# Kernel tuning notes

Hardware: AMD Instinct MI355X
Metric: run time of the kernel (lower is better)

The kernel has to match this reference:

```python
import jax, jax.numpy as jnp
import numpy as np

UP = 2


def _lpf_rect(N, cutoff):
    # ideal lowpass rect over full-FFT frequency axis (with Nyquist 0.5 fix)
    cutoff_low = int((N * cutoff) // 2)
    cutoff_high = int(N - cutoff_low)
    rect = np.ones(N, dtype=np.float32)
    rect[cutoff_low + 1:cutoff_high] = 0.0
    if (N * cutoff) % 2 == 0:
        rect[cutoff_low] = 0.5
        rect[cutoff_high] = 0.5
    return rect


def _recon_rect(N, cutoff):
    # reconstruction rect for zero-insertion upsampling (no Nyquist halving)
    cutoff_low = int((N * cutoff) // 2)
    cutoff_high = int(N - cutoff_low)
    rect = np.ones(N, dtype=np.float32)
    rect[cutoff_low + 1:cutoff_high] = 0.0
    return rect


def _rfft2_mask(rect_h, rect_w):
    # outer product mask on rfft2 grid: full H axis x half W axis
    half_w = rect_w.shape[0] // 2 + 1
    return jnp.asarray(rect_h[:, None] * rect_w[None, :half_w])


def setup_inputs() -> dict:
    key = jax.random.key(0)
    x = jax.random.normal(key, (32, 128, 64, 64), dtype=jnp.float32)
    # PolyAct default init_coef (buffer, non-trainable)
    coef = jnp.array([0.0169394634313126, 0.5, 0.3078363963999393, 0.0],
                     dtype=jnp.float32)
    return {"x": x, "coef": coef}


def reference(x, coef):
    B, C, H, W = x.shape
    Hu, Wu = H * UP, W * UP

    # ---- UpsampleRFFT: zero-insertion then ideal reconstruction filter ----
    xu = jnp.zeros((B, C, Hu, Wu), x.dtype).at[:, :, ::UP, ::UP].set(x)
    recon_mask = _rfft2_mask(_recon_rect(Hu, 1.0 / UP), _recon_rect(Wu, 1.0 / UP))
    f = jnp.fft.rfft2(xu) * (UP * UP) * recon_mask
    xu = jnp.fft.irfft2(f, s=(Hu, Wu))

    # ---- PolyAct: calc_polynomial loops range(2, deg) with deg=3, so only
    # terms up to x^2 are used (coef[3] is never applied) ----
    y = coef[0] + coef[1] * xu + coef[2] * xu * xu

    # ---- LPF_RFFT with cutoff = 1/up ----
    lpf_mask = _rfft2_mask(_lpf_rect(Hu, 1.0 / UP), _lpf_rect(Wu, 1.0 / UP))
    y = jnp.fft.irfft2(jnp.fft.rfft2(y) * lpf_mask, s=(Hu, Wu))

    # ---- decimate back to original resolution ----
    return y[:, :, ::UP, ::UP]
```

## Files before the change

### kernel.cpp

```cpp
#include <hip/hip_runtime.h>
#include <math.h>


typedef short short8 __attribute__((ext_vector_type(8)));
typedef float f32x16 __attribute__((ext_vector_type(16)));

#define LSH 68

__device__ __forceinline__ short f2bf(float f) {
  unsigned u = __float_as_uint(f);
  u += 0x7FFFu + ((u >> 16) & 1u);
  return (short)(u >> 16);
}
__device__ __forceinline__ float bf2f(short s) {
  return __uint_as_float(((unsigned)(unsigned short)s) << 16);
}
__device__ __forceinline__ short8 ldrow(const short* p) {
  union { unsigned u[4]; short8 s; } v;
  const uint2 lo = *(const uint2*)p;
  const uint2 hi = *(const uint2*)(p + 4);
  v.u[0] = lo.x; v.u[1] = lo.y; v.u[2] = hi.x; v.u[3] = hi.y;
  return v.s;
}

__global__ __launch_bounds__(256, 3) void uppolyact_kernel(
    const float* __restrict__ x, const float* __restrict__ coef,
    float* __restrict__ out) {
  __shared__ __align__(16) short Xr[64 * LSH];
  __shared__ __align__(16) short XcZ[64 * LSH];
  __shared__ __align__(16) short LrU[64 * LSH];
  __shared__ __align__(16) short Zoo[64 * LSH];
  __shared__ __align__(16) short ftab[16 * 64 * 8];
  __shared__ float g64[64];
  __shared__ float tvec[64], uvec[64], sRv[64], Luv[64];
  __shared__ float sigv;

  const int tid = threadIdx.x;
  const int lane = tid & 63;
  const int w = tid >> 6;
  const int q = lane >> 5;
  const int l31 = lane & 31;
  const int rb = w >> 1, cb = w & 1;
  const size_t base = (size_t)blockIdx.x * 4096;

  if (tid < 64) {
    const int d = 2 * tid + 1;
    float s = 1.0f;
    for (int k = 1; k <= 32; ++k) {
      const int qq = (k * d) & 127;
      s += 2.0f * cosf((float)M_PI * (1.0f / 64.0f) * (float)qq);
    }
    g64[tid] = s * (1.0f / 64.0f);
  }
  {
    const float4* xv = (const float4*)(x + base);
#pragma unroll
    for (int e = 0; e < 4; ++e) {
      const int k4 = tid + 256 * e;
      const float4 v = xv[k4];
      const int r = k4 >> 4, c = (k4 & 15) << 2;
      const short b0 = f2bf(v.x), b1 = f2bf(v.y), b2 = f2bf(v.z), b3 = f2bf(v.w);
      short* pr = &Xr[r * LSH + c];
      pr[0] = b0; pr[1] = b1; pr[2] = b2; pr[3] = b3;
      XcZ[(c + 0) * LSH + r] = b0;
      XcZ[(c + 1) * LSH + r] = b1;
      XcZ[(c + 2) * LSH + r] = b2;
      XcZ[(c + 3) * LSH + r] = b3;
    }
  }
  __syncthreads();

#pragma unroll
  for (int e = 0; e < 4; ++e) {
    const int entry = tid + 256 * e;
    const int s_ = entry >> 6, ln = entry & 63;
    const int t_ = s_ >> 3, blk = (s_ >> 2) & 1, kk = s_ & 3;
    const int basei = kk * 16 + (ln >> 5) * 8 - (ln & 31) - 32 * blk;
    short* dst = &ftab[(s_ * 64 + ln) * 8];
#pragma unroll
    for (int j = 0; j < 8; ++j) {
      const int i0 = basei + j;
      const int idx = t_ ? ((-i0) & 63) : (i0 & 63);
      dst[j] = f2bf(g64[idx]);
    }
  }
  if (tid < 64) {
    float acc = 0.0f;
    for (int i = 0; i < 64; ++i) {
      const float xv_ = bf2f(XcZ[tid * LSH + i]);
      acc += (i & 1) ? -xv_ : xv_;
    }
    tvec[tid] = acc;
  } else if (tid < 128) {
    const int i = tid - 64;
    float acc = 0.0f;
    for (int j = 0; j < 64; ++j) {
      const float xv_ = bf2f(Xr[i * LSH + j]);
      acc += (j & 1) ? -xv_ : xv_;
    }
    uvec[i] = acc;
  }
  __syncthreads();

  if (tid < 64) {
    float acc = 0.0f;
    for (int m = 0; m < 64; ++m) acc += tvec[m] * g64[(tid - m) & 63];
    sRv[tid] = acc;
  } else if (tid < 128) {
    const int i = tid - 64;
    float acc = 0.0f;
    for (int m = 0; m < 64; ++m) acc += g64[(i - m) & 63] * uvec[m];
    Luv[i] = acc;
  } else if (tid == 128) {
    float acc = 0.0f;
    for (int i = 0; i < 64; ++i) acc += (i & 1) ? -uvec[i] : uvec[i];
    sigv = acc;
  }

  f32x16 Rt, Lt;
#pragma unroll
  for (int r = 0; r < 16; ++r) { Rt[r] = 0.0f; Lt[r] = 0.0f; }
#pragma unroll
  for (int kk = 0; kk < 4; ++kk) {
    const short8 aR = *(const short8*)&ftab[(((2 + rb) * 4 + kk) * 64 + lane) * 8];
    const short8 bR = ldrow(&Xr[(cb * 32 + l31) * LSH + kk * 16 + q * 8]);
    Rt = __builtin_amdgcn_mfma_f32_32x32x16_bf16(aR, bR, Rt, 0, 0, 0);
    const short8 aL = ldrow(&XcZ[(rb * 32 + l31) * LSH + kk * 16 + q * 8]);
    const short8 bL = *(const short8*)&ftab[(((2 + cb) * 4 + kk) * 64 + lane) * 8];
    Lt = __builtin_amdgcn_mfma_f32_32x32x16_bf16(aL, bL, Lt, 0, 0, 0);
  }
  __syncthreads();

  float zoe[16];
#pragma unroll
  for (int r = 0; r < 16; ++r) {
    const int jrow = rb * 32 + (r & 3) + 4 * q + 8 * (r >> 2);
    const int icol = cb * 32 + l31;
    const float sgi = (icol & 1) ? -1.0f : 1.0f;
    const float sgj = (jrow & 1) ? -1.0f : 1.0f;
    const float veo = Rt[r] + sgi * sRv[jrow] * (1.0f / 64.0f);
    XcZ[icol * LSH + jrow] = f2bf(veo * veo);
    LrU[icol * LSH + jrow] = f2bf(Lt[r]);
    const float voe = Lt[r] + Luv[icol] * sgj * (1.0f / 64.0f);
    zoe[r] = voe * voe;
  }
  __syncthreads();

  f32x16 OOt;
#pragma unroll
  for (int r = 0; r < 16; ++r) OOt[r] = 0.0f;
#pragma unroll
  for (int kk = 0; kk < 4; ++kk) {
    const short8 a = *(const short8*)&ftab[(((2 + rb) * 4 + kk) * 64 + lane) * 8];
    const short8 b = ldrow(&LrU[(cb * 32 + l31) * LSH + kk * 16 + q * 8]);
    OOt = __builtin_amdgcn_mfma_f32_32x32x16_bf16(a, b, OOt, 0, 0, 0);
  }
#pragma unroll
  for (int r = 0; r < 16; ++r) {
    const int jrow = rb * 32 + (r & 3) + 4 * q + 8 * (r >> 2);
    const int icol = cb * 32 + l31;
    Zoo[icol * LSH + jrow] = f2bf(OOt[r] * OOt[r]);
  }
  __syncthreads();

  f32x16 Ut, Wv;
#pragma unroll
  for (int r = 0; r < 16; ++r) { Ut[r] = zoe[r]; Wv[r] = 0.0f; }
#pragma unroll
  for (int kk = 0; kk < 4; ++kk) {
    const short8 aU = *(const short8*)&ftab[(((0 + rb) * 4 + kk) * 64 + lane) * 8];
    const short8 bU = ldrow(&Zoo[(cb * 32 + l31) * LSH + kk * 16 + q * 8]);
    Ut = __builtin_amdgcn_mfma_f32_32x32x16_bf16(aU, bU, Ut, 0, 0, 0);
    const short8 aW = ldrow(&XcZ[(rb * 32 + l31) * LSH + kk * 16 + q * 8]);
    const short8 bW = *(const short8*)&ftab[(((0 + cb) * 4 + kk) * 64 + lane) * 8];
    Wv = __builtin_amdgcn_mfma_f32_32x32x16_bf16(aW, bW, Wv, 0, 0, 0);
  }
#pragma unroll
  for (int r = 0; r < 16; ++r) {
    const int jrow = rb * 32 + (r & 3) + 4 * q + 8 * (r >> 2);
    const int icol = cb * 32 + l31;
    LrU[jrow * LSH + icol] = f2bf(Ut[r]);
  }
  __syncthreads();

  f32x16 Vv;
#pragma unroll
  for (int r = 0; r < 16; ++r) Vv[r] = 0.0f;
#pragma unroll
  for (int kk = 0; kk < 4; ++kk) {
    const short8 a = *(const short8*)&ftab[(((0 + rb) * 4 + kk) * 64 + lane) * 8];
    const short8 b = ldrow(&LrU[(cb * 32 + l31) * LSH + kk * 16 + q * 8]);
    Vv = __builtin_amdgcn_mfma_f32_32x32x16_bf16(a, b, Vv, 0, 0, 0);
  }

  const float c0 = coef[0], c1 = coef[1];
  const float c2q = 0.25f * coef[2];
  const float* xb = x + base;
  float* ob = out + base;
#pragma unroll
  for (int r = 0; r < 16; ++r) {
    const int irow = rb * 32 + (r & 3) + 4 * q + 8 * (r >> 2);
    const int jcol = cb * 32 + l31;
    const float sgi = (irow & 1) ? -1.0f : 1.0f;
    const float sgj = (jcol & 1) ? -1.0f : 1.0f;
    const float xv_ = bf2f(Xr[irow * LSH + jcol]);
    const float vee = xv_ + (sgi * tvec[jcol] + uvec[irow] * sgj) * (1.0f / 64.0f) +
                      sgi * sgj * sigv * (1.0f / 4096.0f);
    const float zee = vee * vee;
    const float xg = xb[irow * 64 + jcol];
    ob[irow * 64 + jcol] = c0 + c1 * xg + c2q * (zee + Vv[r] + Wv[r]);
  }
}

extern "C" void kernel_launch(void* const* d_in, const int* in_sizes, int n_in,
                              void* d_out, int out_size, void* d_ws,
                              size_t ws_size, hipStream_t stream) {
  const float* x = (const float*)d_in[0];
  const float* coef = (const float*)d_in[1];
  float* out = (float*)d_out;
  const int channels = out_size / 4096;
  uppolyact_kernel<<<dim3(channels), dim3(256), 0, stream>>>(x, coef, out);
}
```

Measured before the change: 150.4 us.

## Make kernel persistent over channels and parallelize per-channel reductions

The kernel becomes grid-stride persistent: at most 1024 blocks loop over the 4096 channels, so the g64 and ftab twiddle-table setup is paid once per block instead of once per channel. The alternating-sign row and column sums and the circular convolutions are spread across all 256 threads with shuffle reductions, where before only 64 to 128 threads did serial loops. sigv is now computed from tvec through a wave reduction, and the t/u sums overlap with the first MFMA stage. In exchange, each block runs long sequential chains, which can reduce latency hiding between blocks.

```diff
diff --git a/kernel.cpp b/kernel.cpp
--- a/kernel.cpp
+++ b/kernel.cpp
@@ -25,7 +25,7 @@
 
 __global__ __launch_bounds__(256, 3) void uppolyact_kernel(
     const float* __restrict__ x, const float* __restrict__ coef,
-    float* __restrict__ out) {
+    float* __restrict__ out, int nch) {
   __shared__ __align__(16) short Xr[64 * LSH];
   __shared__ __align__(16) short XcZ[64 * LSH];
   __shared__ __align__(16) short LrU[64 * LSH];
@@ -41,7 +41,6 @@
   const int q = lane >> 5;
   const int l31 = lane & 31;
   const int rb = w >> 1, cb = w & 1;
-  const size_t base = (size_t)blockIdx.x * 4096;
 
   if (tid < 64) {
     const int d = 2 * tid + 1;
@@ -52,22 +51,6 @@
     }
     g64[tid] = s * (1.0f / 64.0f);
   }
-  {
-    const float4* xv = (const float4*)(x + base);
-#pragma unroll
-    for (int e = 0; e < 4; ++e) {
-      const int k4 = tid + 256 * e;
-      const float4 v = xv[k4];
-      const int r = k4 >> 4, c = (k4 & 15) << 2;
-      const short b0 = f2bf(v.x), b1 = f2bf(v.y), b2 = f2bf(v.z), b3 = f2bf(v.w);
-      short* pr = &Xr[r * LSH + c];
-      pr[0] = b0; pr[1] = b1; pr[2] = b2; pr[3] = b3;
-      XcZ[(c + 0) * LSH + r] = b0;
-      XcZ[(c + 1) * LSH + r] = b1;
-      XcZ[(c + 2) * LSH + r] = b2;
-      XcZ[(c + 3) * LSH + r] = b3;
-    }
-  }
   __syncthreads();
 
 #pragma unroll
@@ -84,131 +67,167 @@
       dst[j] = f2bf(g64[idx]);
     }
   }
-  if (tid < 64) {
-    float acc = 0.0f;
-    for (int i = 0; i < 64; ++i) {
-      const float xv_ = bf2f(XcZ[tid * LSH + i]);
-      acc += (i & 1) ? -xv_ : xv_;
-    }
-    tvec[tid] = acc;
-  } else if (tid < 128) {
-    const int i = tid - 64;
-    float acc = 0.0f;
-    for (int j = 0; j < 64; ++j) {
-      const float xv_ = bf2f(Xr[i * LSH + j]);
-      acc += (j & 1) ? -xv_ : xv_;
-    }
-    uvec[i] = acc;
-  }
-  __syncthreads();
-
-  if (tid < 64) {
-    float acc = 0.0f;
-    for (int m = 0; m < 64; ++m) acc += tvec[m] * g64[(tid - m) & 63];
-    sRv[tid] = acc;
-  } else if (tid < 128) {
-    const int i = tid - 64;
-    float acc = 0.0f;
-    for (int m = 0; m < 64; ++m) acc += g64[(i - m) & 63] * uvec[m];
-    Luv[i] = acc;
-  } else if (tid == 128) {
-    float acc = 0.0f;
-    for (int i = 0; i < 64; ++i) acc += (i & 1) ? -uvec[i] : uvec[i];
-    sigv = acc;
-  }
-
-  f32x16 Rt, Lt;
-#pragma unroll
-  for (int r = 0; r < 16; ++r) { Rt[r] = 0.0f; Lt[r] = 0.0f; }
-#pragma unroll
-  for (int kk = 0; kk < 4; ++kk) {
-    const short8 aR = *(const short8*)&ftab[(((2 + rb) * 4 + kk) * 64 + lane) * 8];
-    const short8 bR = ldrow(&Xr[(cb * 32 + l31) * LSH + kk * 16 + q * 8]);
-    Rt = __builtin_amdgcn_mfma_f32_32x32x16_bf16(aR, bR, Rt, 0, 0, 0);
-    const short8 aL = ldrow(&XcZ[(rb * 32 + l31) * LSH + kk * 16 + q * 8]);
-    const short8 bL = *(const short8*)&ftab[(((2 + cb) * 4 + kk) * 64 + lane) * 8];
-    Lt = __builtin_amdgcn_mfma_f32_32x32x16_bf16(aL, bL, Lt, 0, 0, 0);
-  }
-  __syncthreads();
-
-  float zoe[16];
-#pragma unroll
-  for (int r = 0; r < 16; ++r) {
-    const int jrow = rb * 32 + (r & 3) + 4 * q + 8 * (r >> 2);
-    const int icol = cb * 32 + l31;
-    const float sgi = (icol & 1) ? -1.0f : 1.0f;
-    const float sgj = (jrow & 1) ? -1.0f : 1.0f;
-    const float veo = Rt[r] + sgi * sRv[jrow] * (1.0f / 64.0f);
-    XcZ[icol * LSH + jrow] = f2bf(veo * veo);
-    LrU[icol * LSH + jrow] = f2bf(Lt[r]);
-    const float voe = Lt[r] + Luv[icol] * sgj * (1.0f / 64.0f);
-    zoe[r] = voe * voe;
-  }
-  __syncthreads();
-
-  f32x16 OOt;
-#pragma unroll
-  for (int r = 0; r < 16; ++r) OOt[r] = 0.0f;
-#pragma unroll
-  for (int kk = 0; kk < 4; ++kk) {
-    const short8 a = *(const short8*)&ftab[(((2 + rb) * 4 + kk) * 64 + lane) * 8];
-    const short8 b = ldrow(&LrU[(cb * 32 + l31) * LSH + kk * 16 + q * 8]);
-    OOt = __builtin_amdgcn_mfma_f32_32x32x16_bf16(a, b, OOt, 0, 0, 0);
-  }
-#pragma unroll
-  for (int r = 0; r < 16; ++r) {
-    const int jrow = rb * 32 + (r & 3) + 4 * q + 8 * (r >> 2);
-    const int icol = cb * 32 + l31;
-    Zoo[icol * LSH + jrow] = f2bf(OOt[r] * OOt[r]);
-  }
-  __syncthreads();
-
-  f32x16 Ut, Wv;
-#pragma unroll
-  for (int r = 0; r < 16; ++r) { Ut[r] = zoe[r]; Wv[r] = 0.0f; }
-#pragma unroll
-  for (int kk = 0; kk < 4; ++kk) {
-    const short8 aU = *(const short8*)&ftab[(((0 + rb) * 4 + kk) * 64 + lane) * 8];
-    const short8 bU = ldrow(&Zoo[(cb * 32 + l31) * LSH + kk * 16 + q * 8]);
-    Ut = __builtin_amdgcn_mfma_f32_32x32x16_bf16(aU, bU, Ut, 0, 0, 0);
-    const short8 aW = ldrow(&XcZ[(rb * 32 + l31) * LSH + kk * 16 + q * 8]);
-    const short8 bW = *(const short8*)&ftab[(((0 + cb) * 4 + kk) * 64 + lane) * 8];
-    Wv = __builtin_amdgcn_mfma_f32_32x32x16_bf16(aW, bW, Wv, 0, 0, 0);
-  }
-#pragma unroll
-  for (int r = 0; r < 16; ++r) {
-    const int jrow = rb * 32 + (r & 3) + 4 * q + 8 * (r >> 2);
-    const int icol = cb * 32 + l31;
-    LrU[jrow * LSH + icol] = f2bf(Ut[r]);
-  }
-  __syncthreads();
-
-  f32x16 Vv;
-#pragma unroll
-  for (int r = 0; r < 16; ++r) Vv[r] = 0.0f;
-#pragma unroll
-  for (int kk = 0; kk < 4; ++kk) {
-    const short8 a = *(const short8*)&ftab[(((0 + rb) * 4 + kk) * 64 + lane) * 8];
-    const short8 b = ldrow(&LrU[(cb * 32 + l31) * LSH + kk * 16 + q * 8]);
-    Vv = __builtin_amdgcn_mfma_f32_32x32x16_bf16(a, b, Vv, 0, 0, 0);
-  }
 
   const float c0 = coef[0], c1 = coef[1];
   const float c2q = 0.25f * coef[2];
-  const float* xb = x + base;
-  float* ob = out + base;
-#pragma unroll
-  for (int r = 0; r < 16; ++r) {
-    const int irow = rb * 32 + (r & 3) + 4 * q + 8 * (r >> 2);
-    const int jcol = cb * 32 + l31;
-    const float sgi = (irow & 1) ? -1.0f : 1.0f;
-    const float sgj = (jcol & 1) ? -1.0f : 1.0f;
-    const float xv_ = bf2f(Xr[irow * LSH + jcol]);
-    const float vee = xv_ + (sgi * tvec[jcol] + uvec[irow] * sgj) * (1.0f / 64.0f) +
-                      sgi * sgj * sigv * (1.0f / 4096.0f);
-    const float zee = vee * vee;
-    const float xg = xb[irow * 64 + jcol];
-    ob[irow * 64 + jcol] = c0 + c1 * xg + c2q * (zee + Vv[r] + Wv[r]);
+
+  for (int ch = blockIdx.x; ch < nch; ch += gridDim.x) {
+    const size_t base = (size_t)ch * 4096;
+    const float* xb = x + base;
+    float* ob = out + base;
+
+    __syncthreads();
+
+    {
+      const float4* xv = (const float4*)xb;
+#pragma unroll
+      for (int e = 0; e < 4; ++e) {
+        const int k4 = tid + 256 * e;
+        const float4 v = xv[k4];
+        const int r = k4 >> 4, c = (k4 & 15) << 2;
+        const short b0 = f2bf(v.x), b1 = f2bf(v.y), b2 = f2bf(v.z), b3 = f2bf(v.w);
+        short* pr = &Xr[r * LSH + c];
+        pr[0] = b0; pr[1] = b1; pr[2] = b2; pr[3] = b3;
+        XcZ[(c + 0) * LSH + r] = b0;
+        XcZ[(c + 1) * LSH + r] = b1;
+        XcZ[(c + 2) * LSH + r] = b2;
+        XcZ[(c + 3) * LSH + r] = b3;
+      }
+    }
+    __syncthreads();
+
+    {
+      const int o = tid >> 1, h = tid & 1;
+      const short* src = (o < 64) ? &XcZ[o * LSH + 32 * h]
+                                  : &Xr[(o - 64) * LSH + 32 * h];
+      float acc = 0.0f;
+#pragma unroll
+      for (int p = 0; p < 4; ++p) {
+        const short8 v = ldrow(src + 8 * p);
+#pragma unroll
+        for (int j = 0; j < 8; ++j) {
+          const float f = bf2f(v[j]);
+          acc += (j & 1) ? -f : f;
+        }
+      }
+      acc += __shfl_xor(acc, 1);
+      if (h == 0) {
+        if (o < 64) tvec[o] = acc; else uvec[o - 64] = acc;
+      }
+    }
+
+    f32x16 Rt, Lt;
+#pragma unroll
+    for (int r = 0; r < 16; ++r) { Rt[r] = 0.0f; Lt[r] = 0.0f; }
+#pragma unroll
+    for (int kk = 0; kk < 4; ++kk) {
+      const short8 aR = *(const short8*)&ftab[(((2 + rb) * 4 + kk) * 64 + lane) * 8];
+      const short8 bR = ldrow(&Xr[(cb * 32 + l31) * LSH + kk * 16 + q * 8]);
+      Rt = __builtin_amdgcn_mfma_f32_32x32x16_bf16(aR, bR, Rt, 0, 0, 0);
+      const short8 aL = ldrow(&XcZ[(rb * 32 + l31) * LSH + kk * 16 + q * 8]);
+      const short8 bL = *(const short8*)&ftab[(((2 + cb) * 4 + kk) * 64 + lane) * 8];
+      Lt = __builtin_amdgcn_mfma_f32_32x32x16_bf16(aL, bL, Lt, 0, 0, 0);
+    }
+    __syncthreads();
+
+    {
+      const int o = tid >> 1, h = tid & 1;
+      const int o63 = o & 63;
+      const float* vsrc = (o < 64) ? tvec : uvec;
+      float acc = 0.0f;
+#pragma unroll
+      for (int p = 0; p < 32; ++p) {
+        const int m = 32 * h + p;
+        acc += vsrc[m] * g64[(o63 - m) & 63];
+      }
+      acc += __shfl_xor(acc, 1);
+      if (h == 0) {
+        if (o < 64) sRv[o] = acc; else Luv[o - 64] = acc;
+      }
+    }
+    if (w == 0) {
+      float sv = (lane & 1) ? -tvec[lane] : tvec[lane];
+#pragma unroll
+      for (int d_ = 1; d_ < 64; d_ <<= 1) sv += __shfl_xor(sv, d_);
+      if (lane == 0) sigv = sv;
+    }
+    __syncthreads();
+
+    float zoe[16];
+#pragma unroll
+    for (int r = 0; r < 16; ++r) {
+      const int jrow = rb * 32 + (r & 3) + 4 * q + 8 * (r >> 2);
+      const int icol = cb * 32 + l31;
+      const float sgi = (icol & 1) ? -1.0f : 1.0f;
+      const float sgj = (jrow & 1) ? -1.0f : 1.0f;
+      const float veo = Rt[r] + sgi * sRv[jrow] * (1.0f / 64.0f);
+      XcZ[icol * LSH + jrow] = f2bf(veo * veo);
+      LrU[icol * LSH + jrow] = f2bf(Lt[r]);
+      const float voe = Lt[r] + Luv[icol] * sgj * (1.0f / 64.0f);
+      zoe[r] = voe * voe;
+    }
+    __syncthreads();
+
+    f32x16 OOt;
+#pragma unroll
+    for (int r = 0; r < 16; ++r) OOt[r] = 0.0f;
+#pragma unroll
+    for (int kk = 0; kk < 4; ++kk) {
+      const short8 a = *(const short8*)&ftab[(((2 + rb) * 4 + kk) * 64 + lane) * 8];
+      const short8 b = ldrow(&LrU[(cb * 32 + l31) * LSH + kk * 16 + q * 8]);
+      OOt = __builtin_amdgcn_mfma_f32_32x32x16_bf16(a, b, OOt, 0, 0, 0);
+    }
+#pragma unroll
+    for (int r = 0; r < 16; ++r) {
+      const int jrow = rb * 32 + (r & 3) + 4 * q + 8 * (r >> 2);
+      const int icol = cb * 32 + l31;
+      Zoo[icol * LSH + jrow] = f2bf(OOt[r] * OOt[r]);
+    }
+    __syncthreads();
+
+    f32x16 Ut, Wv;
+#pragma unroll
+    for (int r = 0; r < 16; ++r) { Ut[r] = zoe[r]; Wv[r] = 0.0f; }
+#pragma unroll
+    for (int kk = 0; kk < 4; ++kk) {
+      const short8 aU = *(const short8*)&ftab[(((0 + rb) * 4 + kk) * 64 + lane) * 8];
+      const short8 bU = ldrow(&Zoo[(cb * 32 + l31) * LSH + kk * 16 + q * 8]);
+      Ut = __builtin_amdgcn_mfma_f32_32x32x16_bf16(aU, bU, Ut, 0, 0, 0);
+      const short8 aW = ldrow(&XcZ[(rb * 32 + l31) * LSH + kk * 16 + q * 8]);
+      const short8 bW = *(const short8*)&ftab[(((0 + cb) * 4 + kk) * 64 + lane) * 8];
+      Wv = __builtin_amdgcn_mfma_f32_32x32x16_bf16(aW, bW, Wv, 0, 0, 0);
+    }
+#pragma unroll
+    for (int r = 0; r < 16; ++r) {
+      const int jrow = rb * 32 + (r & 3) + 4 * q + 8 * (r >> 2);
+      const int icol = cb * 32 + l31;
+      LrU[jrow * LSH + icol] = f2bf(Ut[r]);
+    }
+    __syncthreads();
+
+    f32x16 Vv;
+#pragma unroll
+    for (int r = 0; r < 16; ++r) Vv[r] = 0.0f;
+#pragma unroll
+    for (int kk = 0; kk < 4; ++kk) {
+      const short8 a = *(const short8*)&ftab[(((0 + rb) * 4 + kk) * 64 + lane) * 8];
+      const short8 b = ldrow(&LrU[(cb * 32 + l31) * LSH + kk * 16 + q * 8]);
+      Vv = __builtin_amdgcn_mfma_f32_32x32x16_bf16(a, b, Vv, 0, 0, 0);
+    }
+
+#pragma unroll
+    for (int r = 0; r < 16; ++r) {
+      const int irow = rb * 32 + (r & 3) + 4 * q + 8 * (r >> 2);
+      const int jcol = cb * 32 + l31;
+      const float sgi = (irow & 1) ? -1.0f : 1.0f;
+      const float sgj = (jcol & 1) ? -1.0f : 1.0f;
+      const float xv_ = bf2f(Xr[irow * LSH + jcol]);
+      const float vee = xv_ + (sgi * tvec[jcol] + uvec[irow] * sgj) * (1.0f / 64.0f) +
+                        sgi * sgj * sigv * (1.0f / 4096.0f);
+      const float zee = vee * vee;
+      const float xg = xb[irow * 64 + jcol];
+      ob[irow * 64 + jcol] = c0 + c1 * xg + c2q * (zee + Vv[r] + Wv[r]);
+    }
   }
 }
 
@@ -219,5 +238,7 @@
   const float* coef = (const float*)d_in[1];
   float* out = (float*)d_out;
   const int channels = out_size / 4096;
-  uppolyact_kernel<<<dim3(channels), dim3(256), 0, stream>>>(x, coef, out);
-}
+  int grid = 1024;
+  if (grid > channels) grid = channels;
+  uppolyact_kernel<<<dim3(grid), dim3(256), 0, stream>>>(x, coef, out, channels);
+}
```

After: 233.2 us. 1.55x slower.
